# Optimization experiments

Hardware: AMD Instinct MI355X
Metric: run time of the kernel (lower is better)

## Reference

```python
import jax, jax.numpy as jnp
import numpy as np

B, J, N = 64, 32, 4096
Q_DIM, K_DIM, V_DIM, H = 130, 128, 130, 4


def _init_linear(key, fan_in, fan_out):
    kw, kb = jax.random.split(key)
    bound = 1.0 / np.sqrt(fan_in)
    W = jax.random.uniform(kw, (fan_in, fan_out), jnp.float32, -bound, bound)
    b = jax.random.uniform(kb, (fan_out,), jnp.float32, -bound, bound)
    return W, b


def setup_inputs() -> dict:
    key = jax.random.key(0)
    ks = jax.random.split(key, 10)
    joint_q = jax.random.normal(ks[0], (B, J, Q_DIM), jnp.float32)
    vertex_k = jax.random.normal(ks[1], (B, N, K_DIM), jnp.float32)
    vertex_v = jax.random.normal(ks[2], (B, N, V_DIM), jnp.float32)
    vertex_mask = jax.random.bernoulli(ks[3], 0.1, (B, N))  # True = masked
    # joint_q_encoder: Linear(130,64) ReLU Linear(64, 128*4)
    W1, b1 = _init_linear(ks[4], Q_DIM, 64)
    W2, b2 = _init_linear(ks[5], 64, K_DIM * H)
    # joint_output_layer: Linear(520,64) ReLU Linear(64,32) ReLU Linear(32,1)
    W3, b3 = _init_linear(ks[6], V_DIM * H, 64)
    W4, b4 = _init_linear(ks[7], 64, 32)
    W5, b5 = _init_linear(ks[8], 32, 1)
    return {
        "joint_q": joint_q, "vertex_k": vertex_k, "vertex_v": vertex_v,
        "vertex_mask": vertex_mask,
        "W1": W1, "b1": b1, "W2": W2, "b2": b2,
        "W3": W3, "b3": b3, "W4": W4, "b4": b4, "W5": W5, "b5": b5,
    }


def reference(joint_q, vertex_k, vertex_v, vertex_mask,
              W1, b1, W2, b2, W3, b3, W4, b4, W5, b5):
    b, j, _ = joint_q.shape
    # Encode queries: [B,J,130] -> [B,J,H,K]
    h = jax.nn.relu(joint_q @ W1 + b1)
    q = (h @ W2 + b2).reshape(b, j, H, K_DIM)
    # Attention scores via broadcasted contraction (avoids materializing
    # the expanded K/V copies the torch code builds): [B,J,H,N]
    scores = jnp.einsum('bjhk,bnk->bjhn', q, vertex_k) / np.sqrt(K_DIM).astype(np.float32)
    scores = jnp.where(vertex_mask[:, None, None, :], jnp.float32(-1e9), scores)
    attn = jax.nn.softmax(scores, axis=-1)
    # Weighted values: [B,J,H,V] -> [B,J,H*V]
    out = jnp.einsum('bjhn,bnv->bjhv', attn, vertex_v).reshape(b, j, H * V_DIM)
    # Output MLP -> [B,J]
    out = jax.nn.relu(out @ W3 + b3)
    out = jax.nn.relu(out @ W4 + b4)
    out = (out @ W5 + b5).squeeze(-1)
    return out
```

## Files before the change

kernel.cpp:

```cpp
#include <hip/hip_runtime.h>
#include <hip/hip_bf16.h>

#define BB 64
#define JJ 32
#define NN 4096
#define QD 130
#define KD 128
#define VD 130
#define HH 4
#define CT 8
#define NCH (NN / CT)
#define TIL (NCH / 32)
#define PSTRIDE (JJ + JJ + JJ * VD)

typedef __attribute__((ext_vector_type(8))) __bf16 bf16x8;
typedef __attribute__((ext_vector_type(4))) float  f32x4;

union FW4 { unsigned int u[4]; bf16x8 v; };

#define SEL_HI 0x07060302u

__device__ __forceinline__ unsigned int packhi(float f0, float f1) {
    return __builtin_amdgcn_perm(__float_as_uint(f1), __float_as_uint(f0), SEL_HI);
}
__device__ __forceinline__ float truncbf(float f) {
    return __uint_as_float(__float_as_uint(f) & 0xFFFF0000u);
}
__device__ __forceinline__ void split8(float4 a, float4 b, bf16x8* h, bf16x8* l) {
    FW4 H, L;
    H.u[0] = packhi(a.x, a.y);
    H.u[1] = packhi(a.z, a.w);
    H.u[2] = packhi(b.x, b.y);
    H.u[3] = packhi(b.z, b.w);
    L.u[0] = packhi(a.x - truncbf(a.x), a.y - truncbf(a.y));
    L.u[1] = packhi(a.z - truncbf(a.z), a.w - truncbf(a.w));
    L.u[2] = packhi(b.x - truncbf(b.x), b.y - truncbf(b.y));
    L.u[3] = packhi(b.z - truncbf(b.z), b.w - truncbf(b.w));
    *h = H.v; *l = L.v;
}

__global__ __launch_bounds__(64) void enc_kernel(
        const float* __restrict__ jq,
        const float* __restrict__ W1, const float* __restrict__ b1,
        const float* __restrict__ W2, const float* __restrict__ b2,
        float* __restrict__ qenc) {
    int row = blockIdx.x;
    int t = threadIdx.x;
    __shared__ float x[QD];
    __shared__ float h[64];
    for (int i = t; i < QD; i += 64) x[i] = jq[row * QD + i];
    __syncthreads();
    float a0 = 0.f, a1 = 0.f;
    for (int i = 0; i < QD - 1; i += 2) {
        a0 += x[i] * W1[i * 64 + t];
        a1 += x[i + 1] * W1[(i + 1) * 64 + t];
    }
    h[t] = fmaxf(b1[t] + a0 + a1, 0.f);
    __syncthreads();
    float a[8];
    #pragma unroll
    for (int s = 0; s < 8; ++s) a[s] = b2[t + 64 * s];
    for (int i = 0; i < 64; ++i) {
        float hv = h[i];
        #pragma unroll
        for (int s = 0; s < 8; ++s) a[s] += hv * W2[i * 512 + t + 64 * s];
    }
    #pragma unroll
    for (int s = 0; s < 8; ++s) qenc[row * 512 + t + 64 * s] = a[s];
}

__global__ __launch_bounds__(512, 2) void attn_kernel(
        const float* __restrict__ Kg, const float* __restrict__ Vg,
        const int* __restrict__ maskg, const float* __restrict__ qenc,
        float* __restrict__ part) {
    int blk = blockIdx.x;
    int c = blk & (CT - 1);
    int b = blk / CT;
    int tid = threadIdx.x;
    int wid = tid >> 6;
    int lane = tid & 63;
    int h = wid & 3;
    int qhalf = wid >> 2;
    int g = lane >> 4;
    int q15 = lane & 15;

    __shared__ __align__(16) __bf16 Kf[2][2][2][4][64][8];
    __shared__ __align__(16) __bf16 Vf[2][8][64][8];
    __shared__ float Vt_s[2][32];
    __shared__ int   msks[32];

    int skey = tid >> 4;
    int sdhi = tid & 15;
    int sa = skey >> 3, sb = skey & 7;
    int skh = sb >> 2;
    int sm  = skh ? 4 * (sa ^ 2) + (sb & 3)
                  : 4 * sa + sb;
    int slK = sm + 16 * (sdhi & 3);
    int skst = sdhi >> 2;
    int sv = tid & 127, skb = tid >> 7;
    int svc = sv >> 4;
    int slV = (sv & 15) + 16 * skb;

    const float* Kb = Kg + (size_t)b * NN * KD;
    const float* Vb = Vg + (size_t)b * NN * VD;
    const int*   Mb = maskg + b * NN;

    float4 kfa, kfb;
    float  vf[8];
    float2 vt = {0.f, 0.f};
    int    mk = 0;

    auto sloadK = [&](int T) {
        int n0 = c * NCH + T * 32;
        const float* ks = Kb + (size_t)(n0 + skey) * KD + sdhi * 8;
        kfa = *(const float4*)ks;
        kfb = *(const float4*)(ks + 4);
    };
    auto sloadV = [&](int T) {
        int n0 = c * NCH + T * 32;
        const float* vs = Vb + (size_t)(n0 + skb * 8) * VD + sv;
        #pragma unroll
        for (int j = 0; j < 8; ++j) vf[j] = vs[(size_t)j * VD];
        if (tid < 32) {
            vt = *(const float2*)(Vb + (size_t)(n0 + tid) * VD + 128);
            mk = Mb[n0 + tid];
        }
    };
    auto swriteK = [&](int buf) {
        bf16x8 hh, ll;
        split8(kfa, kfb, &hh, &ll);
        *(bf16x8*)&Kf[buf][0][skh][skst][slK][0] = hh;
        *(bf16x8*)&Kf[buf][1][skh][skst][slK][0] = ll;
    };
    auto swriteV = [&]() {
        bf16x8 hh, ll;
        float4 va = {vf[0], vf[1], vf[2], vf[3]};
        float4 vb2 = {vf[4], vf[5], vf[6], vf[7]};
        split8(va, vb2, &hh, &ll);
        *(bf16x8*)&Vf[0][svc][slV][0] = hh;
        *(bf16x8*)&Vf[1][svc][slV][0] = ll;
        if (tid < 32) {
            Vt_s[0][tid] = vt.x;
            Vt_s[1][tid] = vt.y;
            msks[tid] = mk;
        }
    };

    sloadK(0);
    sloadV(0);

    bf16x8 qh[4], ql[4];
    {
        const float* qrow = qenc + (size_t)(b * JJ + qhalf * 16 + q15) * 512
                            + h * KD + g * 8;
        #pragma unroll
        for (int kst = 0; kst < 4; ++kst) {
            float4 qa = *(const float4*)(qrow + kst * 32);
            float4 qb = *(const float4*)(qrow + kst * 32 + 4);
            split8(qa, qb, &qh[kst], &ql[kst]);
        }
    }

    swriteK(0);
    sloadK(1);
    __builtin_amdgcn_sched_barrier(0);

    f32x4 O[8];
    #pragma unroll
    for (int vc = 0; vc < 8; ++vc)
        #pragma unroll
        for (int r = 0; r < 4; ++r) O[vc][r] = 0.f;
    float acct0 = 0.f, acct1 = 0.f;
    float m_run = -1e30f, l_run = 0.f;

    __syncthreads();

    for (int t = 0; t < TIL; ++t) {
        int cur = t & 1;

        swriteV();
        if (t + 1 < TIL) swriteK(cur ^ 1);
        __builtin_amdgcn_sched_barrier(0);

        f32x4 S[2];
        #pragma unroll
        for (int kh = 0; kh < 2; ++kh)
            #pragma unroll
            for (int r = 0; r < 4; ++r) S[kh][r] = 0.f;
        #pragma unroll
        for (int kst = 0; kst < 4; ++kst) {
            #pragma unroll
            for (int kh = 0; kh < 2; ++kh) {
                bf16x8 khf = *(const bf16x8*)&Kf[cur][0][kh][kst][lane][0];
                bf16x8 klf = *(const bf16x8*)&Kf[cur][1][kh][kst][lane][0];
                S[kh] = __builtin_amdgcn_mfma_f32_16x16x32_bf16(khf, qh[kst], S[kh], 0, 0, 0);
                S[kh] = __builtin_amdgcn_mfma_f32_16x16x32_bf16(khf, ql[kst], S[kh], 0, 0, 0);
                S[kh] = __builtin_amdgcn_mfma_f32_16x16x32_bf16(klf, qh[kst], S[kh], 0, 0, 0);
            }
        }

        __syncthreads();

        if (t + 2 < TIL) sloadK(t + 2);
        if (t + 1 < TIL) sloadV(t + 1);
        __builtin_amdgcn_sched_barrier(0);

        unsigned int mword = (unsigned int)__ballot(msks[lane & 31] != 0);
        const float sc = 0.08838834764831845f;
        float sp[8];
        float rm = -1e30f;
        #pragma unroll
        for (int r = 0; r < 4; ++r) {
            int key0 = 8 * g + r;
            float s0 = ((mword >> key0) & 1u) ? -1e30f : S[0][r] * sc;
            sp[r] = s0;
            rm = fmaxf(rm, s0);
            int key1 = 8 * (g ^ 2) + 4 + r;
            float s1 = ((mword >> key1) & 1u) ? -1e30f : S[1][r] * sc;
            sp[4 + r] = s1;
            rm = fmaxf(rm, s1);
        }
        rm = fmaxf(rm, __shfl_xor(rm, 16));
        rm = fmaxf(rm, __shfl_xor(rm, 32));
        if (!__all(rm <= m_run + 8.f)) {
            float mn = fmaxf(m_run, rm);
            float rs = __expf(m_run - mn);
            m_run = mn;
            l_run *= rs; acct0 *= rs; acct1 *= rs;
            #pragma unroll
            for (int r = 0; r < 4; ++r) {
                float rr = __shfl(rs, g * 4 + r);
                #pragma unroll
                for (int vc = 0; vc < 8; ++vc) O[vc][r] *= rr;
            }
        }
        float ps = 0.f;
        #pragma unroll
        for (int i = 0; i < 8; ++i) {
            float p = __expf(sp[i] - m_run);
            sp[i] = p;
            ps += p;
        }
        ps += __shfl_xor(ps, 16);
        ps += __shfl_xor(ps, 32);
        l_run += ps;

        #pragma unroll
        for (int r = 0; r < 4; ++r) {
            int key0 = 8 * g + r;
            int key1 = 8 * (g ^ 2) + 4 + r;
            acct0 += sp[r] * Vt_s[0][key0] + sp[4 + r] * Vt_s[0][key1];
            acct1 += sp[r] * Vt_s[1][key0] + sp[4 + r] * Vt_s[1][key1];
        }

        unsigned w0h = packhi(sp[0], sp[1]), w1h = packhi(sp[2], sp[3]);
        unsigned w2h = packhi(sp[4], sp[5]), w3h = packhi(sp[6], sp[7]);
        unsigned w0l = packhi(sp[0] - truncbf(sp[0]), sp[1] - truncbf(sp[1]));
        unsigned w1l = packhi(sp[2] - truncbf(sp[2]), sp[3] - truncbf(sp[3]));
        unsigned w2l = packhi(sp[4] - truncbf(sp[4]), sp[5] - truncbf(sp[5]));
        unsigned w3l = packhi(sp[6] - truncbf(sp[6]), sp[7] - truncbf(sp[7]));
        FW4 PH, PL;
        PH.u[0] = w0h; PH.u[1] = w1h;
        PH.u[2] = __shfl_xor(w2h, 32);
        PH.u[3] = __shfl_xor(w3h, 32);
        PL.u[0] = w0l; PL.u[1] = w1l;
        PL.u[2] = __shfl_xor(w2l, 32);
        PL.u[3] = __shfl_xor(w3l, 32);
        bf16x8 PAH = PH.v, PAL = PL.v;

        #pragma unroll
        for (int vc = 0; vc < 8; ++vc) {
            bf16x8 vh = *(const bf16x8*)&Vf[0][vc][lane][0];
            bf16x8 vl = *(const bf16x8*)&Vf[1][vc][lane][0];
            O[vc] = __builtin_amdgcn_mfma_f32_16x16x32_bf16(PAH, vh, O[vc], 0, 0, 0);
            O[vc] = __builtin_amdgcn_mfma_f32_16x16x32_bf16(PAL, vh, O[vc], 0, 0, 0);
            O[vc] = __builtin_amdgcn_mfma_f32_16x16x32_bf16(PAH, vl, O[vc], 0, 0, 0);
        }

        __syncthreads();
    }

    float* P = part + (size_t)((b * HH + h) * CT + c) * PSTRIDE;
    if (lane < 16) {
        P[qhalf * 16 + lane] = m_run;
        P[JJ + qhalf * 16 + lane] = l_run;
    }
    float* A = P + 2 * JJ;
    #pragma unroll
    for (int vc = 0; vc < 8; ++vc) {
        #pragma unroll
        for (int r = 0; r < 4; ++r) {
            int q = qhalf * 16 + g * 4 + r;
            A[q * VD + vc * 16 + q15] = O[vc][r];
        }
    }
    acct0 += __shfl_xor(acct0, 16);
    acct0 += __shfl_xor(acct0, 32);
    acct1 += __shfl_xor(acct1, 16);
    acct1 += __shfl_xor(acct1, 32);
    if (lane < 16) {
        A[(qhalf * 16 + lane) * VD + 128] = acct0;
        A[(qhalf * 16 + lane) * VD + 129] = acct1;
    }
}

__global__ __launch_bounds__(64) void comb_mlp_kernel(
        const float* __restrict__ part,
        const float* __restrict__ W3, const float* __restrict__ b3,
        const float* __restrict__ W4, const float* __restrict__ b4,
        const float* __restrict__ W5, const float* __restrict__ b5,
        float* __restrict__ out) {
    int row = blockIdx.x;
    int b = row >> 5;
    int j = row & 31;
    int t = threadIdx.x;
    __shared__ float w_s[HH][CT];
    __shared__ float x[HH * VD];
    __shared__ float h1[64];
    __shared__ float h2[32];

    if (t < HH * CT) {
        int h = t / CT, cc = t % CT;
        const float* P = part + (size_t)((b * HH + h) * CT + cc) * PSTRIDE;
        float m = P[j];
        float l = P[JJ + j];
        float mm = m;
        #pragma unroll
        for (int s = 1; s < CT; s <<= 1) mm = fmaxf(mm, __shfl_xor(mm, s));
        float e = __expf(m - mm);
        float L = l * e;
        #pragma unroll
        for (int s = 1; s < CT; s <<= 1) L += __shfl_xor(L, s);
        w_s[h][cc] = (L > 0.f) ? e / L : 0.f;
    }
    __syncthreads();

    for (int idx = t; idx < HH * VD; idx += 64) {
        int h = idx / VD, v = idx - h * VD;
        const float* A = part + (size_t)(b * HH + h) * CT * PSTRIDE + 2 * JJ + j * VD + v;
        float o = 0.f;
        #pragma unroll 4
        for (int cc = 0; cc < CT; ++cc) o += w_s[h][cc] * A[(size_t)cc * PSTRIDE];
        x[idx] = o;
    }
    __syncthreads();

    float a0 = 0.f, a1 = 0.f, a2 = 0.f, a3 = 0.f;
    for (int i = 0; i < HH * VD; i += 4) {
        a0 += x[i] * W3[i * 64 + t];
        a1 += x[i + 1] * W3[(i + 1) * 64 + t];
        a2 += x[i + 2] * W3[(i + 2) * 64 + t];
        a3 += x[i + 3] * W3[(i + 3) * 64 + t];
    }
    h1[t] = fmaxf(b3[t] + (a0 + a1) + (a2 + a3), 0.f);
    __syncthreads();
    if (t < 32) {
        float c0 = 0.f, c1 = 0.f;
        for (int i = 0; i < 64; i += 2) {
            c0 += h1[i] * W4[i * 32 + t];
            c1 += h1[i + 1] * W4[(i + 1) * 32 + t];
        }
        h2[t] = fmaxf(b4[t] + c0 + c1, 0.f);
    }
    __syncthreads();
    if (t == 0) {
        float a3f = b5[0];
        for (int i = 0; i < 32; ++i) a3f += h2[i] * W5[i];
        out[row] = a3f;
    }
}

extern "C" void kernel_launch(void* const* d_in, const int* in_sizes, int n_in,
                              void* d_out, int out_size, void* d_ws, size_t ws_size,
                              hipStream_t stream) {
    const float* jq = (const float*)d_in[0];
    const float* Kg = (const float*)d_in[1];
    const float* Vg = (const float*)d_in[2];
    const int* mask = (const int*)d_in[3];
    const float* W1 = (const float*)d_in[4];
    const float* b1 = (const float*)d_in[5];
    const float* W2 = (const float*)d_in[6];
    const float* b2 = (const float*)d_in[7];
    const float* W3 = (const float*)d_in[8];
    const float* b3 = (const float*)d_in[9];
    const float* W4 = (const float*)d_in[10];
    const float* b4 = (const float*)d_in[11];
    const float* W5 = (const float*)d_in[12];
    const float* b5 = (const float*)d_in[13];
    float* out = (float*)d_out;

    float* ws = (float*)d_ws;
    float* qenc = ws;
    float* part = qenc + (size_t)BB * JJ * HH * KD;

    enc_kernel<<<BB * JJ, 64, 0, stream>>>(jq, W1, b1, W2, b2, qenc);
    attn_kernel<<<BB * CT, 512, 0, stream>>>(Kg, Vg, mask, qenc, part);
    comb_mlp_kernel<<<BB * JJ, 64, 0, stream>>>(part, W3, b3, W4, b4, W5, b5, out);
}
```

Measured before the change: 129.7 us.

## Split attention heads across two 256-thread blocks and pad the K shared tile

The attention kernel now launches twice as many blocks of 256 threads, with each block handling two of the four heads instead of all four. Each thread stages two K/V slots to fill the shared tiles, and the launch bounds change to allow three blocks per CU. The K shared-memory tile gains a padding row to change the bank mapping. The aim is more blocks and better latency hiding, but every K/V chunk is now fetched and converted by two blocks, which doubles global/L2 traffic and conversion work.

After: 244.3 us. 88.4% more time.

```diff
diff --git a/kernel.cpp b/kernel.cpp
--- a/kernel.cpp
+++ b/kernel.cpp
@@ -69,58 +69,68 @@
     for (int s = 0; s < 8; ++s) qenc[row * 512 + t + 64 * s] = a[s];
 }
 
-__global__ __launch_bounds__(512, 2) void attn_kernel(
+__global__ __launch_bounds__(256, 3) void attn_kernel(
         const float* __restrict__ Kg, const float* __restrict__ Vg,
         const int* __restrict__ maskg, const float* __restrict__ qenc,
         float* __restrict__ part) {
     int blk = blockIdx.x;
     int c = blk & (CT - 1);
-    int b = blk / CT;
+    int b = (blk >> 3) & (BB - 1);
+    int hg = blk >> 9;
     int tid = threadIdx.x;
     int wid = tid >> 6;
     int lane = tid & 63;
-    int h = wid & 3;
-    int qhalf = wid >> 2;
+    int h = hg * 2 + (wid & 1);
+    int qhalf = wid >> 1;
     int g = lane >> 4;
     int q15 = lane & 15;
 
-    __shared__ __align__(16) __bf16 Kf[2][2][2][4][64][8];
+    __shared__ __align__(16) __bf16 Kf[2][2][2][4][65][8];
     __shared__ __align__(16) __bf16 Vf[2][8][64][8];
     __shared__ float Vt_s[2][32];
     __shared__ int   msks[32];
 
-    int skey = tid >> 4;
-    int sdhi = tid & 15;
-    int sa = skey >> 3, sb = skey & 7;
-    int skh = sb >> 2;
-    int sm  = skh ? 4 * (sa ^ 2) + (sb & 3)
-                  : 4 * sa + sb;
-    int slK = sm + 16 * (sdhi & 3);
-    int skst = sdhi >> 2;
-    int sv = tid & 127, skb = tid >> 7;
-    int svc = sv >> 4;
-    int slV = (sv & 15) + 16 * skb;
+    int p0 = tid, p1 = tid + 256;
+    int skey0 = p0 >> 4, sdhi0 = p0 & 15;
+    int skey1 = p1 >> 4, sdhi1 = p1 & 15;
+    int sa0 = skey0 >> 3, sb0 = skey0 & 7;
+    int sa1 = skey1 >> 3, sb1 = skey1 & 7;
+    int skh0 = sb0 >> 2, skh1 = sb1 >> 2;
+    int sm0 = skh0 ? 4 * (sa0 ^ 2) + (sb0 & 3) : 4 * sa0 + sb0;
+    int sm1 = skh1 ? 4 * (sa1 ^ 2) + (sb1 & 3) : 4 * sa1 + sb1;
+    int slK0 = sm0 + 16 * (sdhi0 & 3), skst0 = sdhi0 >> 2;
+    int slK1 = sm1 + 16 * (sdhi1 & 3), skst1 = sdhi1 >> 2;
+    int sv0 = p0 & 127, skb0 = p0 >> 7;
+    int sv1 = p1 & 127, skb1 = p1 >> 7;
+    int svc0 = sv0 >> 4, slV0 = (sv0 & 15) + 16 * skb0;
+    int svc1 = sv1 >> 4, slV1 = (sv1 & 15) + 16 * skb1;
 
     const float* Kb = Kg + (size_t)b * NN * KD;
     const float* Vb = Vg + (size_t)b * NN * VD;
     const int*   Mb = maskg + b * NN;
 
-    float4 kfa, kfb;
-    float  vf[8];
+    float4 kfa0, kfb0, kfa1, kfb1;
+    float  vf0[8], vf1[8];
     float2 vt = {0.f, 0.f};
     int    mk = 0;
 
     auto sloadK = [&](int T) {
         int n0 = c * NCH + T * 32;
-        const float* ks = Kb + (size_t)(n0 + skey) * KD + sdhi * 8;
-        kfa = *(const float4*)ks;
-        kfb = *(const float4*)(ks + 4);
+        const float* ks0 = Kb + (size_t)(n0 + skey0) * KD + sdhi0 * 8;
+        kfa0 = *(const float4*)ks0;
+        kfb0 = *(const float4*)(ks0 + 4);
+        const float* ks1 = Kb + (size_t)(n0 + skey1) * KD + sdhi1 * 8;
+        kfa1 = *(const float4*)ks1;
+        kfb1 = *(const float4*)(ks1 + 4);
     };
     auto sloadV = [&](int T) {
         int n0 = c * NCH + T * 32;
-        const float* vs = Vb + (size_t)(n0 + skb * 8) * VD + sv;
-        #pragma unroll
-        for (int j = 0; j < 8; ++j) vf[j] = vs[(size_t)j * VD];
+        const float* vs0 = Vb + (size_t)(n0 + skb0 * 8) * VD + sv0;
+        #pragma unroll
+        for (int j = 0; j < 8; ++j) vf0[j] = vs0[(size_t)j * VD];
+        const float* vs1 = Vb + (size_t)(n0 + skb1 * 8) * VD + sv1;
+        #pragma unroll
+        for (int j = 0; j < 8; ++j) vf1[j] = vs1[(size_t)j * VD];
         if (tid < 32) {
             vt = *(const float2*)(Vb + (size_t)(n0 + tid) * VD + 128);
             mk = Mb[n0 + tid];
@@ -128,17 +138,25 @@
     };
     auto swriteK = [&](int buf) {
         bf16x8 hh, ll;
-        split8(kfa, kfb, &hh, &ll);
-        *(bf16x8*)&Kf[buf][0][skh][skst][slK][0] = hh;
-        *(bf16x8*)&Kf[buf][1][skh][skst][slK][0] = ll;
+        split8(kfa0, kfb0, &hh, &ll);
+        *(bf16x8*)&Kf[buf][0][skh0][skst0][slK0][0] = hh;
+        *(bf16x8*)&Kf[buf][1][skh0][skst0][slK0][0] = ll;
+        split8(kfa1, kfb1, &hh, &ll);
+        *(bf16x8*)&Kf[buf][0][skh1][skst1][slK1][0] = hh;
+        *(bf16x8*)&Kf[buf][1][skh1][skst1][slK1][0] = ll;
     };
     auto swriteV = [&]() {
         bf16x8 hh, ll;
-        float4 va = {vf[0], vf[1], vf[2], vf[3]};
-        float4 vb2 = {vf[4], vf[5], vf[6], vf[7]};
+        float4 va = {vf0[0], vf0[1], vf0[2], vf0[3]};
+        float4 vb2 = {vf0[4], vf0[5], vf0[6], vf0[7]};
         split8(va, vb2, &hh, &ll);
-        *(bf16x8*)&Vf[0][svc][slV][0] = hh;
-        *(bf16x8*)&Vf[1][svc][slV][0] = ll;
+        *(bf16x8*)&Vf[0][svc0][slV0][0] = hh;
+        *(bf16x8*)&Vf[1][svc0][slV0][0] = ll;
+        float4 vc3 = {vf1[0], vf1[1], vf1[2], vf1[3]};
+        float4 vd = {vf1[4], vf1[5], vf1[6], vf1[7]};
+        split8(vc3, vd, &hh, &ll);
+        *(bf16x8*)&Vf[0][svc1][slV1][0] = hh;
+        *(bf16x8*)&Vf[1][svc1][slV1][0] = ll;
         if (tid < 32) {
             Vt_s[0][tid] = vt.x;
             Vt_s[1][tid] = vt.y;
@@ -394,6 +412,6 @@
     float* part = qenc + (size_t)BB * JJ * HH * KD;
 
     enc_kernel<<<BB * JJ, 64, 0, stream>>>(jq, W1, b1, W2, b2, qenc);
-    attn_kernel<<<BB * CT, 512, 0, stream>>>(Kg, Vg, mask, qenc, part);
+    attn_kernel<<<BB * CT * 2, 256, 0, stream>>>(Kg, Vg, mask, qenc, part);
     comb_mlp_kernel<<<BB * JJ, 64, 0, stream>>>(part, W3, b3, W4, b4, W5, b5, out);
 }
```
